# Kernel optimization log

Hardware: AMD Instinct MI355X
Metric: run time of the kernel (lower is better)

The kernel has to match this reference:

```python
import jax, jax.numpy as jnp
import numpy as np

P, N, M, B = 5, 30000, 50000, 256
T, C, L, ED, H, EMB, TD, NL = 13, 16, 3, 4, 128, 64, 5, 3
SRC = jnp.repeat(jnp.arange(P), P)  # edge type i = src*P + dst
DST = jnp.tile(jnp.arange(P), P)


def _affine(x, W, b):
    # x: [P, n, i], W: [P, i, o], b: [P, o]
    return jnp.einsum('pni,pio->pno', x, W) + b[:, None, :]


def _lrelu(x, s=0.01):
    return jnp.where(x >= 0, x, s * x)


def _gat(h, W, a_s, a_d, We, a_e, b, edge_index, edge_attr):
    # h: [P, N, H]; per-edge-type GATConv (heads=1, no self loops) then hetero 'max' aggregation
    hs, hd = h[SRC], h[DST]                       # [25, N, H]
    xl = jnp.einsum('enh,ehf->enf', hs, W)        # transformed source features
    xr = jnp.einsum('enh,ehf->enf', hd, W)
    als = jnp.einsum('enf,ef->en', xl, a_s)
    ald = jnp.einsum('enf,ef->en', xr, a_d)

    def per_type(xl_e, als_e, ald_e, ea, We_e, ae_e, ei):
        src, dst = ei[0], ei[1]
        alpha = als_e[src] + ald_e[dst] + (ea @ We_e) @ ae_e
        alpha = jnp.where(alpha >= 0, alpha, 0.2 * alpha)  # GAT negative_slope=0.2
        amax = jax.ops.segment_max(alpha, dst, num_segments=N)
        ex = jnp.exp(alpha - amax[dst])
        den = jax.ops.segment_sum(ex, dst, num_segments=N)
        w = ex / (den[dst] + 1e-16)
        return jax.ops.segment_sum(w[:, None] * xl_e[src], dst, num_segments=N)

    out = jax.vmap(per_type)(xl, als, ald, edge_attr, We, a_e, edge_index)
    out = out + b[:, None, :]
    return out.reshape(P, P, N, H).max(axis=0)  # HeteroConv aggr='max' over source types


def setup_inputs():
    key = jax.random.key(0)
    ks = iter(jax.random.split(key, 64))
    def nrm(shape, s=1.0):
        return jax.random.normal(next(ks), shape, dtype=jnp.float32) * s
    w = 0.05
    inp = {
        'x': nrm((P, N, T)),
        'cond_x': nrm((P, N, C + L)),
        'edge_attr': nrm((P * P, M, ED)),
        'timesteps': jax.random.uniform(next(ks), (B,), dtype=jnp.float32),
        'te1_W': nrm((1, TD), w), 'te1_b': nrm((TD,), w),
        'te2_W': nrm((TD, TD), w), 'te2_b': nrm((TD,), w),
        'emb_W': nrm((P, T + L, EMB), w), 'emb_b': nrm((P, EMB), w),
        'cemb_W': nrm((P, C, EMB), w), 'cemb_b': nrm((P, EMB), w),
        'pa_W': nrm((P, 2 * EMB, 2 * EMB), w), 'pa_b': nrm((P, 2 * EMB), w),
        'pc_W': nrm((P, 2 * EMB, EMB), w), 'pc_b': nrm((P, EMB), w),
        'sl0_W': nrm((P, EMB + TD, H), w), 'sl0_b': nrm((P, H), w),
        'sl12_W': nrm((2, P, H + TD, H), w), 'sl12_b': nrm((2, P, H), w),
        'slout_W': nrm((P, H + TD, T), w), 'slout_b': nrm((P, T), w),
        'gat_W': nrm((NL, P * P, H, H), w), 'gat_as': nrm((NL, P * P, H), w),
        'gat_ad': nrm((NL, P * P, H), w), 'gat_We': nrm((NL, P * P, ED, H), w),
        'gat_ae': nrm((NL, P * P, H), w), 'gat_b': nrm((NL, P * P, H), w),
        'xc_W': nrm((NL, P, H, H // 2), w), 'xc_b': nrm((NL, P, H // 2), w),
        'cc_W': nrm((NL, P, H, H // 2), w), 'cc_b': nrm((NL, P, H // 2), w),
        'ca_W': nrm((NL, P, H, H), w), 'ca_b': nrm((NL, P, H), w),
        'batch_idx': jax.random.randint(next(ks), (P, N), 0, B),
        'edge_index': jax.random.randint(next(ks), (P * P, 2, M), 0, N),
    }
    return inp


def reference(x, cond_x, edge_attr, timesteps, te1_W, te1_b, te2_W, te2_b,
              emb_W, emb_b, cemb_W, cemb_b, pa_W, pa_b, pc_W, pc_b,
              sl0_W, sl0_b, sl12_W, sl12_b, slout_W, slout_b,
              gat_W, gat_as, gat_ad, gat_We, gat_ae, gat_b,
              xc_W, xc_b, cc_W, cc_b, ca_W, ca_b, batch_idx, edge_index):
    # time embedding: Linear(1,TD) -> SiLU -> Linear(TD,TD)
    temb = jax.nn.silu(timesteps[:, None] @ te1_W + te1_b) @ te2_W + te2_b  # [B, TD]
    cond, latent = cond_x[..., :C], cond_x[..., C:]
    h = _affine(jnp.concatenate([x, latent], -1), emb_W, emb_b)            # [P,N,EMB]
    ce = _affine(cond, cemb_W, cemb_b)
    h = jnp.concatenate([h, ce], -1)                                       # [P,N,2EMB]
    h = jax.nn.sigmoid(_affine(h, pa_W, pa_b)) * h                         # attention pooling
    h = _affine(h, pc_W, pc_b)                                             # [P,N,EMB]
    nt = temb[batch_idx]                                                   # [P,N,TD]
    h = jnp.concatenate([h, nt], -1)
    for l in range(NL):
        if l > 0:
            h = jnp.concatenate([h, nt], -1)
        Wl, bl = (sl0_W, sl0_b) if l == 0 else (sl12_W[l - 1], sl12_b[l - 1])
        h = _lrelu(_affine(h, Wl, bl))                                     # [P,N,H]
        comm = _lrelu(_gat(h, gat_W[l], gat_as[l], gat_ad[l], gat_We[l], gat_ae[l], gat_b[l], edge_index, edge_attr))
        h = jnp.concatenate([_affine(h, xc_W[l], xc_b[l]), _affine(comm, cc_W[l], cc_b[l])], -1)
        h = h + jax.nn.sigmoid(_affine(h, ca_W[l], ca_b[l])) * h
    h = jnp.concatenate([h, nt], -1)
    return _affine(h, slout_W, slout_b)                                    # [P,N,T]
```

## Files before the change

kernel.cpp:

```cpp
#include <hip/hip_runtime.h>
#include <cstdio>

using bf8 = __attribute__((ext_vector_type(8))) short;
using f4v = __attribute__((ext_vector_type(4))) float;
typedef unsigned short u16;
typedef unsigned int u32;

#define DEV __device__ __forceinline__

DEV float bf2f(u16 u){ return __uint_as_float(((u32)u) << 16); }
DEV u16 f2bf(float f){ u32 u = __float_as_uint(f); return (u16)((u + 0x7fffu + ((u >> 16) & 1u)) >> 16); }
DEV float sigm(float v){ return 1.f / (1.f + __expf(-v)); }

constexpr int P5 = 5, NN = 30000, MM = 50000, NE = 25, BB = 256;
constexpr int KC = 96;
constexpr int RS = KC * 2 + 16;
constexpr int RSA = 272;

__global__ void temb_k(const float* ts, const float* w1, const float* b1,
                       const float* w2, const float* b2, float* temb){
  int i = blockIdx.x * blockDim.x + threadIdx.x;
  if (i >= BB) return;
  float t = ts[i]; float z[5];
#pragma unroll
  for (int j = 0; j < 5; ++j){ float u = t * w1[j] + b1[j]; z[j] = u * sigm(u); }
#pragma unroll
  for (int j2 = 0; j2 < 5; ++j2){
    float s = b2[j2];
#pragma unroll
    for (int j = 0; j < 5; ++j) s += z[j] * w2[j * 5 + j2];
    temb[i * 5 + j2] = s;
  }
}

__global__ void wtransE_k(const float* __restrict__ W, u16* __restrict__ Wt,
                          int Kreal, int Kpad, int Nreal, int Nalloc, int total){
  int idx = blockIdx.x * blockDim.x + threadIdx.x;
  if (idx >= total) return;
  int k = idx % Kpad;
  int t2 = idx / Kpad;
  int f = t2 % Nalloc;
  int b = t2 / Nalloc;
  float v = (k < Kreal && f < Nreal) ? W[((size_t)b * Kreal + k) * Nreal + f] : 0.f;
  Wt[idx] = f2bf(v);
}

__global__ void embw_k(const float* emb_W, const float* emb_b, const float* cemb_W, const float* cemb_b,
                       u16* Wc, float* bc){
  int b = blockIdx.x, f = threadIdx.x;
  for (int k = 0; k < 32; ++k){
    float v = 0.f;
    if (f < 64){ if (k < 16) v = emb_W[((size_t)b * 16 + k) * 64 + f]; }
    else       { if (k >= 16) v = cemb_W[((size_t)b * 16 + (k - 16)) * 64 + (f - 64)]; }
    Wc[((size_t)b * 128 + f) * 32 + k] = f2bf(v);
  }
  bc[b * 128 + f] = (f < 64) ? emb_b[b * 64 + f] : cemb_b[b * 64 + (f - 64)];
}

__global__ void gwtT_k(const float* __restrict__ gW, u16* __restrict__ gWt){
  int idx = blockIdx.x * blockDim.x + threadIdx.x;
  if (idx >= 75 * 128 * 128) return;
  int h = idx & 127, f = (idx >> 7) & 127, le = idx >> 14;
  gWt[idx] = f2bf(gW[(size_t)le * 16384 + h * 128 + f]);
}

__global__ void gatred_k(const float* gW, const float* gas, const float* gad,
                         const float* gWe, const float* gae,
                         float* wswd, float* eaw){
  int le = blockIdx.x; int h = threadIdx.x;
  const float* W = gW + (size_t)le * 16384;
  const float* as_ = gas + le * 128;
  const float* ad_ = gad + le * 128;
  float wsv = 0.f, wdv = 0.f;
  for (int f = 0; f < 128; ++f){
    float w = W[h * 128 + f];
    wsv += w * as_[f]; wdv += w * ad_[f];
  }
  wswd[le * 256 + h] = wsv;
  wswd[le * 256 + 128 + h] = wdv;
  if (h < 4){
    const float* We = gWe + (size_t)le * 512;
    const float* ae = gae + le * 128;
    float s = 0.f;
    for (int f = 0; f < 128; ++f) s += We[h * 128 + f] * ae[f];
    eaw[le * 4 + h] = s;
  }
}

__global__ void abuild_k(const float* x, const float* cx, u16* A0){
  int idx = blockIdx.x * blockDim.x + threadIdx.x;
  if (idx >= P5 * NN) return;
  const float* xr = x + (size_t)idx * 13;
  const float* cr = cx + (size_t)idx * 19;
  u16* a0 = A0 + (size_t)idx * 32;
#pragma unroll
  for (int i = 0; i < 13; ++i) a0[i] = f2bf(xr[i]);
#pragma unroll
  for (int i = 0; i < 3; ++i) a0[13 + i] = f2bf(cr[16 + i]);
#pragma unroll
  for (int i = 0; i < 16; ++i) a0[16 + i] = f2bf(cr[i]);
}

__global__ void ntfill_k(u16* buf, int pitch, int co, const int* bidx, const float* temb){
  int idx = blockIdx.x * blockDim.x + threadIdx.x;
  if (idx >= P5 * NN) return;
  int b = bidx[idx];
  u16* r = buf + (size_t)idx * pitch;
#pragma unroll
  for (int j = 0; j < 5; ++j) r[co + j] = f2bf(temb[b * 5 + j]);
  for (int j = co + 5; j < pitch; ++j) r[j] = 0;
}

__global__ __launch_bounds__(1024) void csr_build_k(const int* __restrict__ EI, int* __restrict__ off,
                                                    int* __restrict__ mpos, int* __restrict__ srcC){
  extern __shared__ int cntl[];
  __shared__ int wsum[16];
  int e = blockIdx.x, tid = threadIdx.x;
  int lane = tid & 63, wv = tid >> 6;
  for (int i = tid; i < NN; i += 1024) cntl[i] = 0;
  __syncthreads();
  const int* srcp = EI + (size_t)e * 2 * MM;
  const int* dstp = srcp + MM;
  for (int m = tid; m < MM; m += 1024) atomicAdd(&cntl[dstp[m]], 1);
  __syncthreads();
  int running = 0;
  for (int c = 0; c < 30; ++c){
    int idx = c * 1024 + tid;
    int v = (idx < NN) ? cntl[idx] : 0;
    int s = v;
#pragma unroll
    for (int o = 1; o < 64; o <<= 1){ int t = __shfl_up(s, o, 64); if (lane >= o) s += t; }
    if (lane == 63) wsum[wv] = s;
    __syncthreads();
    if (wv == 0 && lane < 16){
      int t = wsum[lane];
#pragma unroll
      for (int o = 1; o < 16; o <<= 1){ int u = __shfl_up(t, o, 64); if (lane >= o) t += u; }
      wsum[lane] = t;
    }
    __syncthreads();
    int base = running + ((wv > 0) ? wsum[wv - 1] : 0);
    int ex = base + s - v;
    if (idx < NN){ off[(size_t)e * (NN + 1) + idx] = ex; cntl[idx] = ex; }
    running += wsum[15];
    __syncthreads();
  }
  if (tid == 0) off[(size_t)e * (NN + 1) + NN] = running;
  __syncthreads();
  for (int m = tid; m < MM; m += 1024){
    int d = dstp[m];
    int pos = atomicAdd(&cntl[d], 1);
    mpos[(size_t)e * MM + m] = pos;
    srcC[(size_t)e * MM + pos] = srcp[m];
  }
}

__global__ void eadot_k(const float* __restrict__ ea, const float* __restrict__ eaw,
                        const int* __restrict__ mpos, float* __restrict__ eadot){
  int idx = blockIdx.x * blockDim.x + threadIdx.x;
  if (idx >= 3 * NE * MM) return;
  int l = idx / (NE * MM);
  int rem = idx - l * NE * MM;
  int e = rem / MM, m = rem - e * MM;
  const float* a4 = ea + ((size_t)e * MM + m) * 4;
  const float* ew = eaw + (size_t)(l * NE + e) * 4;
  float d = a4[0] * ew[0] + a4[1] * ew[1] + a4[2] * ew[2] + a4[3] * ew[3];
  eadot[(size_t)l * NE * MM + (size_t)e * MM + mpos[rem]] = d;
}

__global__ __launch_bounds__(256) void dots2_k(const u16* __restrict__ hS, const float* __restrict__ wswd_l,
                                               float* __restrict__ als, float* __restrict__ ald){
  __shared__ u32 hl[64][65];
  __shared__ float wsl[10][129];
  int p = blockIdx.y;
  int n0 = blockIdx.x * 64;
  int tid = threadIdx.x;
  for (int i = tid; i < 10 * 128; i += 256){
    int col = i >> 7, k = i & 127;
    int e = (col < 5) ? (p * 5 + col) : ((col - 5) * 5 + p);
    wsl[col][k] = wswd_l[e * 256 + ((col < 5) ? 0 : 128) + k];
  }
  for (int i = tid; i < 64 * 64; i += 256){
    int r = i >> 6, kp = i & 63;
    int n = n0 + r;
    hl[r][kp] = (n < NN) ? ((const u32*)hS)[((size_t)p * NN + n) * 64 + kp] : 0u;
  }
  __syncthreads();
  int col = tid & 15, rbase = tid >> 4;
  if (col < 10){
#pragma unroll
    for (int pass = 0; pass < 4; ++pass){
      int r = rbase + pass * 16;
      int n = n0 + r;
      if (n >= NN) continue;
      float s = 0.f;
#pragma unroll
      for (int kp = 0; kp < 64; ++kp){
        u32 pr = hl[r][kp];
        s += bf2f((u16)(pr & 0xffffu)) * wsl[col][2 * kp]
           + bf2f((u16)(pr >> 16)) * wsl[col][2 * kp + 1];
      }
      if (col < 5) als[(size_t)(p * 5 + col) * NN + n] = s;
      else         ald[(size_t)((col - 5) * 5 + p) * NN + n] = s;
    }
  }
}

__global__ __launch_bounds__(256) void aexp_k(const float* __restrict__ als, const float* __restrict__ ald,
                                              const float* __restrict__ eadot_l, const int* __restrict__ srcC,
                                              const int* __restrict__ off, uint2* __restrict__ prec){
  int idx = blockIdx.x * blockDim.x + threadIdx.x;
  if (idx >= NE * NN) return;
  int e = idx / NN;
  int ro = off[(size_t)e + idx], re = off[(size_t)e + idx + 1];
  if (ro >= re) return;
  float av = ald[idx];
  const int* sc = srcC + (size_t)e * MM;
  const float* ed = eadot_l + (size_t)e * MM;
  const float* ale = als + (size_t)e * NN;
  float mx = -3.0e38f;
  for (int j = ro; j < re; ++j){
    float a = ale[sc[j]] + av + ed[j];
    a = (a >= 0.f) ? a : 0.2f * a;
    mx = fmaxf(mx, a);
  }
  for (int j = ro; j < re; ++j){
    int src = sc[j];
    float a = ale[src] + av + ed[j];
    a = (a >= 0.f) ? a : 0.2f * a;
    uint2 pr; pr.x = (u32)src; pr.y = __float_as_uint(__expf(a - mx));
    prec[(size_t)e * MM + j] = pr;
  }
}

__global__ __launch_bounds__(256) void agg3_k(const u16* __restrict__ hS, const uint2* __restrict__ prec,
                                              const int* __restrict__ off, u16* __restrict__ agghB,
                                              int pd0, int npd){
  int l = threadIdx.x & 63, w = threadIdx.x >> 6;
  int n0 = blockIdx.x * 8 + w;
  int n1 = n0 + 4;
  int y = blockIdx.y;
  int ps = y / npd, e = ps * 5 + pd0 + (y - ps * npd);
  const uint2* pe = prec + (size_t)e * MM;
  const int* offe = off + (size_t)e * (NN + 1);
  const u32* hb = (const u32*)hS + (size_t)ps * NN * 64 + l;
  int ro0 = 0, ln0 = 0, ro1 = 0, ln1 = 0;
  if (n0 < NN){ ro0 = offe[n0]; ln0 = offe[n0 + 1] - ro0; }
  if (n1 < NN){ ro1 = offe[n1]; ln1 = offe[n1 + 1] - ro1; }
  float den0 = 0.f, a00 = 0.f, a01 = 0.f;
  float den1 = 0.f, a10 = 0.f, a11 = 0.f;
  int mx = (ln0 > ln1) ? ln0 : ln1;
  for (int t = 0; t < mx; ++t){
    if (t < ln0){
      uint2 pr = pe[ro0 + t];
      float ex = __uint_as_float(pr.y);
      u32 hv = hb[(size_t)pr.x * 64];
      den0 += ex; a00 += ex * bf2f((u16)(hv & 0xffffu)); a01 += ex * bf2f((u16)(hv >> 16));
    }
    if (t < ln1){
      uint2 pr = pe[ro1 + t];
      float ex = __uint_as_float(pr.y);
      u32 hv = hb[(size_t)pr.x * 64];
      den1 += ex; a10 += ex * bf2f((u16)(hv & 0xffffu)); a11 += ex * bf2f((u16)(hv >> 16));
    }
  }
  if (n0 < NN){
    float inv = 1.f / (den0 + 1e-16f);
    ((u32*)agghB)[((size_t)y * NN + n0) * 64 + l] = (u32)f2bf(a00 * inv) | ((u32)f2bf(a01 * inv) << 16);
  }
  if (n1 < NN){
    float inv = 1.f / (den1 + 1e-16f);
    ((u32*)agghB)[((size_t)y * NN + n1) * 64 + l] = (u32)f2bf(a10 * inv) | ((u32)f2bf(a11 * inv) << 16);
  }
}

template<int NF, int MI, int NJ, int EPI, bool ALRELU>
__global__ __launch_bounds__(256) void tgemm_k(const u16* __restrict__ A, const u16* __restrict__ Wt,
                                               const float* __restrict__ bias, void* __restrict__ out,
                                               const u16* __restrict__ X,
                                               int Kpad, int opitch, int ocol, int xpitch){
  constexpr int Nalloc = NF * 16;
  constexpr int WR = 128 / (MI * 16);
  constexpr int WC = 4 / WR;
  static_assert(WR * WC == 4 && NJ * WC * 16 == Nalloc, "wave tiling");
  extern __shared__ __align__(16) char smem[];
  float* Cs = (float*)smem;
  const int tid = threadIdx.x;
  const int l = tid & 63, w = tid >> 6;
  const int bz = blockIdx.z;
  const int r0 = blockIdx.x * 128;
  const int wr = w / WC, wc = w % WC;
  const size_t Ab = (size_t)bz * NN;

  f4v acc[MI][NJ];
#pragma unroll
  for (int i = 0; i < MI; ++i)
#pragma unroll
    for (int j = 0; j < NJ; ++j) acc[i][j] = f4v{0.f, 0.f, 0.f, 0.f};

  for (int kb = 0; kb < Kpad; kb += KC){
    int kc = Kpad - kb; if (kc > KC) kc = KC;
    int nseg = kc >> 3;
    for (int s = tid; s < 128 * nseg; s += 256){
      int r = s / nseg, c = s - r * nseg;
      int grow = r0 + r; if (grow > NN - 1) grow = NN - 1;
      uint4 v = *(const uint4*)(A + (Ab + grow) * Kpad + kb + c * 8);
      if (ALRELU){
        u32 pr[4] = {v.x, v.y, v.z, v.w};
#pragma unroll
        for (int q = 0; q < 4; ++q){
          float lo = bf2f((u16)(pr[q] & 0xffffu)), hi = bf2f((u16)(pr[q] >> 16));
          lo = lo >= 0.f ? lo : 0.01f * lo; hi = hi >= 0.f ? hi : 0.01f * hi;
          pr[q] = (u32)f2bf(lo) | ((u32)f2bf(hi) << 16);
        }
        v.x = pr[0]; v.y = pr[1]; v.z = pr[2]; v.w = pr[3];
      }
      *(uint4*)(smem + r * RS + c * 16) = v;
    }
    for (int s = tid; s < Nalloc * nseg; s += 256){
      int r = s / nseg, c = s - r * nseg;
      uint4 v = *(const uint4*)(Wt + ((size_t)bz * Nalloc + r) * Kpad + kb + c * 8);
      *(uint4*)(smem + 128 * RS + r * RS + c * 16) = v;
    }
    __syncthreads();
    int KI = kc >> 5;
    for (int k0 = 0; k0 < KI; ++k0){
      bf8 af[MI], bfr[NJ];
#pragma unroll
      for (int i = 0; i < MI; ++i){
        int row = wr * (MI * 16) + i * 16 + (l & 15);
        af[i] = *(const bf8*)(smem + row * RS + k0 * 64 + (l >> 4) * 16);
      }
#pragma unroll
      for (int j = 0; j < NJ; ++j){
        int col = wc * (NJ * 16) + j * 16 + (l & 15);
        bfr[j] = *(const bf8*)(smem + 128 * RS + col * RS + k0 * 64 + (l >> 4) * 16);
      }
#pragma unroll
      for (int i = 0; i < MI; ++i)
#pragma unroll
        for (int j = 0; j < NJ; ++j)
          acc[i][j] = __builtin_amdgcn_mfma_f32_16x16x32_bf16(af[i], bfr[j], acc[i][j], 0, 0, 0);
    }
    __syncthreads();
  }

  if (EPI == 4){
    int col = l & 15;
    if (col < 13){
#pragma unroll
      for (int i = 0; i < MI; ++i){
        float bv = bias[bz * 13 + col];
#pragma unroll
        for (int r = 0; r < 4; ++r){
          int grow = r0 + wr * (MI * 16) + i * 16 + (l >> 4) * 4 + r;
          if (grow < NN)
            ((float*)out)[((size_t)bz * NN + grow) * 13 + col] = acc[i][0][r] + bv;
        }
      }
    }
    return;
  }

#pragma unroll
  for (int i = 0; i < MI; ++i)
#pragma unroll
    for (int j = 0; j < NJ; ++j){
      int tcol = wc * (NJ * 16) + j * 16 + (l & 15);
      float bv = bias[bz * Nalloc + tcol];
#pragma unroll
      for (int r = 0; r < 4; ++r){
        int trow = wr * (MI * 16) + i * 16 + (l >> 4) * 4 + r;
        float v = acc[i][j][r] + bv;
        if (EPI == 2) v = v >= 0.f ? v : 0.01f * v;
        Cs[trow * Nalloc + tcol] = v;
      }
    }
  __syncthreads();
  constexpr int nsc = Nalloc / 4;
  u16* o16 = (u16*)out;
  for (int s = tid; s < 128 * nsc; s += 256){
    int r = s / nsc, c = s - r * nsc;
    int grow = r0 + r; if (grow >= NN) continue;
    float4 cv = *(const float4*)(Cs + r * Nalloc + c * 4);
    float v0 = cv.x, v1 = cv.y, v2 = cv.z, v3 = cv.w;
    if (EPI == 1){
      uint2 xv = *(const uint2*)(X + ((size_t)bz * NN + grow) * xpitch + c * 4);
      float x0 = bf2f((u16)(xv.x & 0xffffu)), x1 = bf2f((u16)(xv.x >> 16));
      float x2 = bf2f((u16)(xv.y & 0xffffu)), x3 = bf2f((u16)(xv.y >> 16));
      v0 = x0 * sigm(v0); v1 = x1 * sigm(v1); v2 = x2 * sigm(v2); v3 = x3 * sigm(v3);
    }
    uint2 ov;
    ov.x = (u32)f2bf(v0) | ((u32)f2bf(v1) << 16);
    ov.y = (u32)f2bf(v2) | ((u32)f2bf(v3) << 16);
    *(uint2*)(o16 + ((size_t)bz * NN + grow) * opitch + ocol + c * 4) = ov;
  }
}

__global__ __launch_bounds__(256) void tgatmm_k(const u16* __restrict__ agghB, const u16* __restrict__ gWt_l,
                                                const float* __restrict__ gb_l, u16* __restrict__ comm,
                                                int pd){
  extern __shared__ __align__(16) char smem[];
  char* As = smem;
  char* Bs = smem + 128 * RSA;
  float* Cs = (float*)smem;
  const int tid = threadIdx.x, l = tid & 63, w = tid >> 6;
  const int r0 = blockIdx.x * 128;
  const int wr = w >> 1, wc = w & 1;
  f4v vmax[4][4];
#pragma unroll 1
  for (int ps = 0; ps < 5; ++ps){
    int e = ps * 5 + pd;
    const u16* aggs = agghB + (size_t)ps * NN * 128;
    const u16* wb = gWt_l + (size_t)e * 16384;
    for (int s = tid; s < 128 * 16; s += 256){
      int r = s >> 4, c = s & 15;
      int grow = r0 + r; if (grow > NN - 1) grow = NN - 1;
      *(uint4*)(As + r * RSA + c * 16) = *(const uint4*)(aggs + (size_t)grow * 128 + c * 8);
      *(uint4*)(Bs + r * RSA + c * 16) = *(const uint4*)(wb + r * 128 + c * 8);
    }
    __syncthreads();
    f4v acc[4][4];
#pragma unroll
    for (int i = 0; i < 4; ++i)
#pragma unroll
      for (int j = 0; j < 4; ++j) acc[i][j] = f4v{0.f, 0.f, 0.f, 0.f};
#pragma unroll
    for (int k0 = 0; k0 < 4; ++k0){
      bf8 af[4], bfr[4];
#pragma unroll
      for (int i = 0; i < 4; ++i)
        af[i] = *(const bf8*)(As + (wr * 64 + i * 16 + (l & 15)) * RSA + k0 * 64 + (l >> 4) * 16);
#pragma unroll
      for (int j = 0; j < 4; ++j)
        bfr[j] = *(const bf8*)(Bs + (wc * 64 + j * 16 + (l & 15)) * RSA + k0 * 64 + (l >> 4) * 16);
#pragma unroll
      for (int i = 0; i < 4; ++i)
#pragma unroll
        for (int j = 0; j < 4; ++j)
          acc[i][j] = __builtin_amdgcn_mfma_f32_16x16x32_bf16(af[i], bfr[j], acc[i][j], 0, 0, 0);
    }
    const float* be = gb_l + e * 128;
#pragma unroll
    for (int i = 0; i < 4; ++i)
#pragma unroll
      for (int j = 0; j < 4; ++j){
        int tcol = wc * 64 + j * 16 + (l & 15);
        float bv = be[tcol];
#pragma unroll
        for (int r = 0; r < 4; ++r){
          float cvv = acc[i][j][r] + bv;
          vmax[i][j][r] = (ps == 0) ? cvv : fmaxf(vmax[i][j][r], cvv);
        }
      }
    __syncthreads();
  }
#pragma unroll
  for (int i = 0; i < 4; ++i)
#pragma unroll
    for (int j = 0; j < 4; ++j){
      int tcol = wc * 64 + j * 16 + (l & 15);
#pragma unroll
      for (int r = 0; r < 4; ++r){
        int trow = wr * 64 + i * 16 + (l >> 4) * 4 + r;
        Cs[trow * 128 + tcol] = vmax[i][j][r];
      }
    }
  __syncthreads();
  for (int s = tid; s < 128 * 32; s += 256){
    int r = s >> 5, c = s & 31;
    int grow = r0 + r; if (grow >= NN) continue;
    float4 cv = *(const float4*)(Cs + r * 128 + c * 4);
    uint2 ov;
    ov.x = (u32)f2bf(cv.x) | ((u32)f2bf(cv.y) << 16);
    ov.y = (u32)f2bf(cv.z) | ((u32)f2bf(cv.w) << 16);
    *(uint2*)(comm + ((size_t)pd * NN + grow) * 128 + c * 4) = ov;
  }
}

__global__ __launch_bounds__(512) void fca_k(const u16* __restrict__ hS, const u16* __restrict__ comm,
                                             const u16* __restrict__ wxc_l, const float* __restrict__ bxc_l,
                                             const u16* __restrict__ wcc_l, const float* __restrict__ bcc_l,
                                             const u16* __restrict__ wca_l, const float* __restrict__ bca_l,
                                             u16* __restrict__ hL){
  extern __shared__ __align__(16) char smem[];
  char* As = smem;
  char* H2 = smem + 128 * RSA;
  const int tid = threadIdx.x, l = tid & 63, wv = tid >> 6;
  const int wr = wv >> 1, wc = wv & 1;
  const int bz = blockIdx.z;
  const int r0 = blockIdx.x * 128;
  const size_t pb = (size_t)bz * NN;

  f4v acc_a[2][2], acc_b[2][2];
  for (int s = tid; s < 128 * 16; s += 512){
    int r = s >> 4, c = s & 15;
    int grow = r0 + r; if (grow > NN - 1) grow = NN - 1;
    *(uint4*)(As + r * RSA + c * 16) = *(const uint4*)(hS + (pb + grow) * 128 + c * 8);
  }
  for (int s = tid; s < 64 * 16; s += 512){
    int r = s >> 4, c = s & 15;
    *(uint4*)(H2 + r * RSA + c * 16) = *(const uint4*)(wxc_l + (size_t)bz * 8192 + r * 128 + c * 8);
  }
  __syncthreads();
#pragma unroll
  for (int i = 0; i < 2; ++i)
#pragma unroll
    for (int j = 0; j < 2; ++j) acc_a[i][j] = f4v{0.f, 0.f, 0.f, 0.f};
#pragma unroll
  for (int k0 = 0; k0 < 4; ++k0){
    bf8 af[2], bfr[2];
#pragma unroll
    for (int i = 0; i < 2; ++i)
      af[i] = *(const bf8*)(As + (wr * 32 + i * 16 + (l & 15)) * RSA + k0 * 64 + (l >> 4) * 16);
#pragma unroll
    for (int j = 0; j < 2; ++j)
      bfr[j] = *(const bf8*)(H2 + (wc * 32 + j * 16 + (l & 15)) * RSA + k0 * 64 + (l >> 4) * 16);
#pragma unroll
    for (int i = 0; i < 2; ++i)
#pragma unroll
      for (int j = 0; j < 2; ++j)
        acc_a[i][j] = __builtin_amdgcn_mfma_f32_16x16x32_bf16(af[i], bfr[j], acc_a[i][j], 0, 0, 0);
  }
  __syncthreads();
  for (int s = tid; s < 128 * 16; s += 512){
    int r = s >> 4, c = s & 15;
    int grow = r0 + r; if (grow > NN - 1) grow = NN - 1;
    uint4 v = *(const uint4*)(comm + (pb + grow) * 128 + c * 8);
    u32 pr[4] = {v.x, v.y, v.z, v.w};
#pragma unroll
    for (int q = 0; q < 4; ++q){
      float lo = bf2f((u16)(pr[q] & 0xffffu)), hi = bf2f((u16)(pr[q] >> 16));
      lo = lo >= 0.f ? lo : 0.01f * lo; hi = hi >= 0.f ? hi : 0.01f * hi;
      pr[q] = (u32)f2bf(lo) | ((u32)f2bf(hi) << 16);
    }
    v.x = pr[0]; v.y = pr[1]; v.z = pr[2]; v.w = pr[3];
    *(uint4*)(As + r * RSA + c * 16) = v;
  }
  for (int s = tid; s < 64 * 16; s += 512){
    int r = s >> 4, c = s & 15;
    *(uint4*)(H2 + r * RSA + c * 16) = *(const uint4*)(wcc_l + (size_t)bz * 8192 + r * 128 + c * 8);
  }
  __syncthreads();
#pragma unroll
  for (int i = 0; i < 2; ++i)
#pragma unroll
    for (int j = 0; j < 2; ++j) acc_b[i][j] = f4v{0.f, 0.f, 0.f, 0.f};
#pragma unroll
  for (int k0 = 0; k0 < 4; ++k0){
    bf8 af[2], bfr[2];
#pragma unroll
    for (int i = 0; i < 2; ++i)
      af[i] = *(const bf8*)(As + (wr * 32 + i * 16 + (l & 15)) * RSA + k0 * 64 + (l >> 4) * 16);
#pragma unroll
    for (int j = 0; j < 2; ++j)
      bfr[j] = *(const bf8*)(H2 + (wc * 32 + j * 16 + (l & 15)) * RSA + k0 * 64 + (l >> 4) * 16);
#pragma unroll
    for (int i = 0; i < 2; ++i)
#pragma unroll
      for (int j = 0; j < 2; ++j)
        acc_b[i][j] = __builtin_amdgcn_mfma_f32_16x16x32_bf16(af[i], bfr[j], acc_b[i][j], 0, 0, 0);
  }
  __syncthreads();
#pragma unroll
  for (int i = 0; i < 2; ++i)
#pragma unroll
    for (int j = 0; j < 2; ++j){
      int colL = wc * 32 + j * 16 + (l & 15);
      float bL = bxc_l[bz * 64 + colL];
      float bR = bcc_l[bz * 64 + colL];
#pragma unroll
      for (int r = 0; r < 4; ++r){
        int row = wr * 32 + i * 16 + (l >> 4) * 4 + r;
        *(u16*)(H2 + row * RSA + colL * 2)       = f2bf(acc_a[i][j][r] + bL);
        *(u16*)(H2 + row * RSA + (colL + 64) * 2) = f2bf(acc_b[i][j][r] + bR);
      }
    }
  for (int s = tid; s < 128 * 16; s += 512){
    int r = s >> 4, c = s & 15;
    *(uint4*)(As + r * RSA + c * 16) = *(const uint4*)(wca_l + (size_t)bz * 16384 + r * 128 + c * 8);
  }
  __syncthreads();
  f4v acc_g[2][4];
#pragma unroll
  for (int i = 0; i < 2; ++i)
#pragma unroll
    for (int j = 0; j < 4; ++j) acc_g[i][j] = f4v{0.f, 0.f, 0.f, 0.f};
#pragma unroll
  for (int k0 = 0; k0 < 4; ++k0){
    bf8 af[2], bfr[4];
#pragma unroll
    for (int i = 0; i < 2; ++i)
      af[i] = *(const bf8*)(H2 + (wr * 32 + i * 16 + (l & 15)) * RSA + k0 * 64 + (l >> 4) * 16);
#pragma unroll
    for (int j = 0; j < 4; ++j)
      bfr[j] = *(const bf8*)(As + (wc * 64 + j * 16 + (l & 15)) * RSA + k0 * 64 + (l >> 4) * 16);
#pragma unroll
    for (int i = 0; i < 2; ++i)
#pragma unroll
      for (int j = 0; j < 4; ++j)
        acc_g[i][j] = __builtin_amdgcn_mfma_f32_16x16x32_bf16(af[i], bfr[j], acc_g[i][j], 0, 0, 0);
  }
  float vout[2][4][4];
#pragma unroll
  for (int i = 0; i < 2; ++i)
#pragma unroll
    for (int j = 0; j < 4; ++j){
      int col = wc * 64 + j * 16 + (l & 15);
      float bv = bca_l[bz * 128 + col];
#pragma unroll
      for (int r = 0; r < 4; ++r){
        int row = wr * 32 + i * 16 + (l >> 4) * 4 + r;
        float xg = bf2f(*(const u16*)(H2 + row * RSA + col * 2));
        vout[i][j][r] = xg * (1.f + sigm(acc_g[i][j][r] + bv));
      }
    }
  __syncthreads();
#pragma unroll
  for (int i = 0; i < 2; ++i)
#pragma unroll
    for (int j = 0; j < 4; ++j){
      int col = wc * 64 + j * 16 + (l & 15);
#pragma unroll
      for (int r = 0; r < 4; ++r){
        int row = wr * 32 + i * 16 + (l >> 4) * 4 + r;
        *(u16*)(H2 + row * RSA + col * 2) = f2bf(vout[i][j][r]);
      }
    }
  __syncthreads();
  for (int s = tid; s < 128 * 32; s += 512){
    int r = s >> 5, c = s & 31;
    int grow = r0 + r; if (grow >= NN) continue;
    uint2 v = *(const uint2*)(H2 + r * RSA + c * 8);
    *(uint2*)(hL + (pb + grow) * 160 + c * 4) = v;
  }
}

constexpr size_t ALN(size_t x){ return (x + 255) & ~(size_t)255; }
constexpr size_t SZ_A0   = ALN((size_t)P5 * NN * 32 * 2);
constexpr size_t SZ_H0   = ALN((size_t)P5 * NN * 96 * 2);
constexpr size_t SZ_H128 = ALN((size_t)P5 * NN * 128 * 2);
constexpr size_t SZ_HL   = ALN((size_t)P5 * NN * 160 * 2);
constexpr size_t O_A0 = 0;
constexpr size_t O_H0 = O_A0 + SZ_A0;
constexpr size_t O_AGG = 0;
constexpr size_t O_HCAT = O_H0 + SZ_H0;
constexpr size_t O_HG = O_HCAT + SZ_H128;
constexpr size_t O_HS = O_HG + SZ_H128;
constexpr size_t O_HL = O_HS + SZ_H128;
constexpr size_t O_TEMB = O_HL + SZ_HL;
constexpr size_t O_WSWD = O_TEMB + ALN(256 * 5 * 4);
constexpr size_t O_EAW  = O_WSWD + ALN(75 * 256 * 4);
constexpr size_t O_OFFS = O_EAW + ALN(75 * 4 * 4);
constexpr size_t O_MPOS = O_OFFS + ALN((size_t)NE * (NN + 1) * 4);
constexpr size_t O_ALS  = O_MPOS + ALN((size_t)NE * MM * 4);
constexpr size_t O_ALD  = O_ALS + ALN((size_t)NE * NN * 4);
constexpr size_t O_SRCC = O_ALD + ALN((size_t)NE * NN * 4);
constexpr size_t O_EADOT= O_SRCC + ALN((size_t)NE * MM * 4);
constexpr size_t O_GWT  = O_EADOT + ALN((size_t)3 * NE * MM * 4);
constexpr size_t O_WCMB = O_GWT + ALN((size_t)75 * 16384 * 2);
constexpr size_t O_BCMB = O_WCMB + ALN((size_t)5 * 128 * 32 * 2);
constexpr size_t O_WPA  = O_BCMB + ALN((size_t)5 * 128 * 4);
constexpr size_t O_WPC  = O_WPA + ALN((size_t)5 * 128 * 128 * 2);
constexpr size_t O_WSL0 = O_WPC + ALN((size_t)5 * 64 * 128 * 2);
constexpr size_t O_WSL12= O_WSL0 + ALN((size_t)5 * 128 * 96 * 2);
constexpr size_t O_WSLO = O_WSL12 + ALN((size_t)10 * 128 * 160 * 2);
constexpr size_t O_WXC  = O_WSLO + ALN((size_t)5 * 16 * 160 * 2);
constexpr size_t O_WCC  = O_WXC + ALN((size_t)15 * 64 * 128 * 2);
constexpr size_t O_WCA  = O_WCC + ALN((size_t)15 * 64 * 128 * 2);
constexpr size_t O_PREC = O_WCA + ALN((size_t)15 * 128 * 128 * 2);
constexpr size_t WS_NEED= O_PREC + ALN((size_t)NE * MM * 8);

extern "C" void kernel_launch(void* const* d_in, const int* in_sizes, int n_in,
                              void* d_out, int out_size, void* d_ws, size_t ws_size,
                              hipStream_t stream){
  if (ws_size < WS_NEED){
    fprintf(stderr, "kernel_launch: ws too small: need %zu have %zu\n", WS_NEED, ws_size);
    return;
  }
  const float* x        = (const float*)d_in[0];
  const float* cond_x   = (const float*)d_in[1];
  const float* edge_attr= (const float*)d_in[2];
  const float* timesteps= (const float*)d_in[3];
  const float* te1_W = (const float*)d_in[4];
  const float* te1_b = (const float*)d_in[5];
  const float* te2_W = (const float*)d_in[6];
  const float* te2_b = (const float*)d_in[7];
  const float* emb_W = (const float*)d_in[8];
  const float* emb_b = (const float*)d_in[9];
  const float* cemb_W= (const float*)d_in[10];
  const float* cemb_b= (const float*)d_in[11];
  const float* pa_W  = (const float*)d_in[12];
  const float* pa_b  = (const float*)d_in[13];
  const float* pc_W  = (const float*)d_in[14];
  const float* pc_b  = (const float*)d_in[15];
  const float* sl0_W = (const float*)d_in[16];
  const float* sl0_b = (const float*)d_in[17];
  const float* sl12_W= (const float*)d_in[18];
  const float* sl12_b= (const float*)d_in[19];
  const float* slout_W=(const float*)d_in[20];
  const float* slout_b=(const float*)d_in[21];
  const float* gat_W = (const float*)d_in[22];
  const float* gat_as= (const float*)d_in[23];
  const float* gat_ad= (const float*)d_in[24];
  const float* gat_We= (const float*)d_in[25];
  const float* gat_ae= (const float*)d_in[26];
  const float* gat_b = (const float*)d_in[27];
  const float* xc_W  = (const float*)d_in[28];
  const float* xc_b  = (const float*)d_in[29];
  const float* cc_W  = (const float*)d_in[30];
  const float* cc_b  = (const float*)d_in[31];
  const float* ca_W  = (const float*)d_in[32];
  const float* ca_b  = (const float*)d_in[33];
  const int* batch_idx = (const int*)d_in[34];
  const int* edge_index= (const int*)d_in[35];

  char* ws = (char*)d_ws;
  u16* A0    = (u16*)(ws + O_A0);
  u16* h0buf = (u16*)(ws + O_H0);
  u16* agghB = (u16*)(ws + O_AGG);
  u16* hcat  = (u16*)(ws + O_HCAT);
  u16* hg    = (u16*)(ws + O_HG);
  u16* comm  = (u16*)(ws + O_HG);
  u16* hS    = (u16*)(ws + O_HS);
  u16* hL    = (u16*)(ws + O_HL);
  float* tembp = (float*)(ws + O_TEMB);
  float* wswdp = (float*)(ws + O_WSWD);
  float* eawp  = (float*)(ws + O_EAW);
  int* offs = (int*)(ws + O_OFFS);
  int* mposp= (int*)(ws + O_MPOS);
  float* alsp = (float*)(ws + O_ALS);
  float* aldp = (float*)(ws + O_ALD);
  int* srcCp = (int*)(ws + O_SRCC);
  float* eadotp = (float*)(ws + O_EADOT);
  u16* gwt   = (u16*)(ws + O_GWT);
  u16* wcmb  = (u16*)(ws + O_WCMB);
  float* bcmb= (float*)(ws + O_BCMB);
  u16* wpa   = (u16*)(ws + O_WPA);
  u16* wpc   = (u16*)(ws + O_WPC);
  u16* wsl0  = (u16*)(ws + O_WSL0);
  u16* wsl12 = (u16*)(ws + O_WSL12);
  u16* wslo  = (u16*)(ws + O_WSLO);
  u16* wxc   = (u16*)(ws + O_WXC);
  u16* wcc   = (u16*)(ws + O_WCC);
  u16* wca   = (u16*)(ws + O_WCA);
  uint2* precp = (uint2*)(ws + O_PREC);

  const dim3 B256(256);
  const dim3 TG(235, 1, 5);
  const int GPN = (P5 * NN + 255) / 256;
  const int GEN = (NE * NN + 255) / 256;
  constexpr int LDS_N128 = 65536;
  constexpr int LDS_N64  = 39936;
  constexpr int LDS_SLO  = 29952;
  constexpr int LDS_TGAT = 128 * RSA * 2;
  constexpr int LDS_FCA  = 128 * RSA * 2;
  constexpr int LDS_CSR  = NN * 4;

  temb_k<<<1, B256, 0, stream>>>(timesteps, te1_W, te1_b, te2_W, te2_b, tembp);
  embw_k<<<5, 128, 0, stream>>>(emb_W, emb_b, cemb_W, cemb_b, wcmb, bcmb);
  {
    auto WT = [&](const float* W, u16* Wt, int Kr, int Kp, int Nr, int Na, int B){
      int total = B * Na * Kp;
      wtransE_k<<<(total + 255) / 256, B256, 0, stream>>>(W, Wt, Kr, Kp, Nr, Na, total);
    };
    WT(pa_W, wpa, 128, 128, 128, 128, 5);
    WT(pc_W, wpc, 128, 128, 64, 64, 5);
    WT(sl0_W, wsl0, 69, 96, 128, 128, 5);
    WT(sl12_W, wsl12, 133, 160, 128, 128, 10);
    WT(slout_W, wslo, 133, 160, 13, 16, 5);
    WT(xc_W, wxc, 128, 128, 64, 64, 15);
    WT(cc_W, wcc, 128, 128, 64, 64, 15);
    WT(ca_W, wca, 128, 128, 128, 128, 15);
  }
  gwtT_k<<<(75 * 128 * 128 + 255) / 256, B256, 0, stream>>>(gat_W, gwt);
  gatred_k<<<75, 128, 0, stream>>>(gat_W, gat_as, gat_ad, gat_We, gat_ae, wswdp, eawp);

  csr_build_k<<<25, 1024, LDS_CSR, stream>>>(edge_index, offs, mposp, srcCp);
  eadot_k<<<(3 * NE * MM + 255) / 256, B256, 0, stream>>>(edge_attr, eawp, mposp, eadotp);

  abuild_k<<<GPN, B256, 0, stream>>>(x, cond_x, A0);
  tgemm_k<8, 4, 4, 0, false><<<TG, B256, LDS_N128, stream>>>(A0, wcmb, bcmb, hcat, nullptr, 32, 128, 0, 0);
  tgemm_k<8, 4, 4, 1, false><<<TG, B256, LDS_N128, stream>>>(hcat, wpa, pa_b, hg, hcat, 128, 128, 0, 128);
  tgemm_k<4, 2, 4, 0, false><<<TG, B256, LDS_N64, stream>>>(hg, wpc, pc_b, h0buf, nullptr, 128, 96, 0, 0);
  ntfill_k<<<GPN, B256, 0, stream>>>(h0buf, 96, 64, batch_idx, tembp);

  for (int l = 0; l < 3; ++l){
    if (l == 0)
      tgemm_k<8, 4, 4, 2, false><<<TG, B256, LDS_N128, stream>>>(h0buf, wsl0, sl0_b, hS, nullptr, 96, 128, 0, 0);
    else
      tgemm_k<8, 4, 4, 2, false><<<TG, B256, LDS_N128, stream>>>(hL, wsl12 + (size_t)(l - 1) * 5 * 128 * 160,
                                                                 sl12_b + (size_t)(l - 1) * 5 * 128, hS, nullptr,
                                                                 160, 128, 0, 0);
    const float* wswd_l = wswdp + (size_t)l * 25 * 256;
    const u16* gwt_l = gwt + (size_t)l * 25 * 16384;
    const float* gb_l = gat_b + (size_t)l * 25 * 128;
    dots2_k<<<dim3(469, 5), B256, 0, stream>>>(hS, wswd_l, alsp, aldp);
    aexp_k<<<GEN, B256, 0, stream>>>(alsp, aldp, eadotp + (size_t)l * NE * MM, srcCp, offs, precp);
    for (int pd = 0; pd < 5; ++pd){
      agg3_k<<<dim3(3750, 5), B256, 0, stream>>>(hS, precp, offs, agghB, pd, 1);
      tgatmm_k<<<dim3(235), B256, LDS_TGAT, stream>>>(agghB, gwt_l, gb_l, comm, pd);
    }
    fca_k<<<dim3(235, 1, 5), 512, LDS_FCA, stream>>>(hS, comm,
        wxc + (size_t)l * 5 * 64 * 128, xc_b + (size_t)l * 5 * 64,
        wcc + (size_t)l * 5 * 64 * 128, cc_b + (size_t)l * 5 * 64,
        wca + (size_t)l * 5 * 128 * 128, ca_b + (size_t)l * 5 * 128, hL);
    ntfill_k<<<GPN, B256, 0, stream>>>(hL, 160, 128, batch_idx, tembp);
  }

  tgemm_k<1, 2, 1, 4, false><<<TG, B256, LDS_SLO, stream>>>(hL, wslo, slout_b, d_out, nullptr, 160, 13, 0, 0);
}
```

Before: 1.821 ms.

## Fuse edge-attr dot into CSR build, halve tgatmm tiles, fuse ntfill into fca

The edge-attribute dot products are now computed inside csr_build_k at the scatter position, which removes the mpos buffer and the separate eadot kernel. The CSR prefix scan becomes a single-pass per-thread serial scan over 30 counts each. tgatmm_k now uses 64-row tiles with twice as many blocks, for better occupancy on 256 CUs. The time-embedding fill of hL is folded into the fca epilogue, dropping three ntfill launches. The serial per-thread scan gives strided LDS access, and the smaller GEMM tiles reload the weight tile more often.

```diff
diff --git a/kernel.cpp b/kernel.cpp
--- a/kernel.cpp
+++ b/kernel.cpp
@@ -111,8 +111,10 @@
   for (int j = co + 5; j < pitch; ++j) r[j] = 0;
 }
 
-__global__ __launch_bounds__(1024) void csr_build_k(const int* __restrict__ EI, int* __restrict__ off,
-                                                    int* __restrict__ mpos, int* __restrict__ srcC){
+__global__ __launch_bounds__(1024) void csr_build_k(const int* __restrict__ EI, const float* __restrict__ ea,
+                                                    const float* __restrict__ eaw,
+                                                    int* __restrict__ off, int* __restrict__ srcC,
+                                                    float* __restrict__ eadot){
   extern __shared__ int cntl[];
   __shared__ int wsum[16];
   int e = blockIdx.x, tid = threadIdx.x;
@@ -123,49 +125,44 @@
   const int* dstp = srcp + MM;
   for (int m = tid; m < MM; m += 1024) atomicAdd(&cntl[dstp[m]], 1);
   __syncthreads();
-  int running = 0;
-  for (int c = 0; c < 30; ++c){
-    int idx = c * 1024 + tid;
-    int v = (idx < NN) ? cntl[idx] : 0;
-    int s = v;
-#pragma unroll
-    for (int o = 1; o < 64; o <<= 1){ int t = __shfl_up(s, o, 64); if (lane >= o) s += t; }
-    if (lane == 63) wsum[wv] = s;
-    __syncthreads();
-    if (wv == 0 && lane < 16){
-      int t = wsum[lane];
-#pragma unroll
-      for (int o = 1; o < 16; o <<= 1){ int u = __shfl_up(t, o, 64); if (lane >= o) t += u; }
-      wsum[lane] = t;
-    }
-    __syncthreads();
-    int base = running + ((wv > 0) ? wsum[wv - 1] : 0);
-    int ex = base + s - v;
-    if (idx < NN){ off[(size_t)e * (NN + 1) + idx] = ex; cntl[idx] = ex; }
-    running += wsum[15];
-    __syncthreads();
-  }
-  if (tid == 0) off[(size_t)e * (NN + 1) + NN] = running;
-  __syncthreads();
+  int t0 = tid * 30, t1 = t0 + 30;
+  if (t0 > NN) t0 = NN;
+  if (t1 > NN) t1 = NN;
+  int tsum = 0;
+  for (int i = t0; i < t1; ++i) tsum += cntl[i];
+  int s = tsum;
+#pragma unroll
+  for (int o = 1; o < 64; o <<= 1){ int t = __shfl_up(s, o, 64); if (lane >= o) s += t; }
+  if (lane == 63) wsum[wv] = s;
+  __syncthreads();
+  if (wv == 0 && lane < 16){
+    int t = wsum[lane];
+#pragma unroll
+    for (int o = 1; o < 16; o <<= 1){ int u = __shfl_up(t, o, 64); if (lane >= o) t += u; }
+    wsum[lane] = t;
+  }
+  __syncthreads();
+  int run = ((wv > 0) ? wsum[wv - 1] : 0) + (s - tsum);
+  for (int i = t0; i < t1; ++i){
+    int v = cntl[i];
+    off[(size_t)e * (NN + 1) + i] = run;
+    cntl[i] = run;
+    run += v;
+  }
+  if (tid == 0) off[(size_t)e * (NN + 1) + NN] = wsum[15];
+  __syncthreads();
+  float4 ew0 = *(const float4*)(eaw + (size_t)(0 * NE + e) * 4);
+  float4 ew1 = *(const float4*)(eaw + (size_t)(1 * NE + e) * 4);
+  float4 ew2 = *(const float4*)(eaw + (size_t)(2 * NE + e) * 4);
   for (int m = tid; m < MM; m += 1024){
     int d = dstp[m];
     int pos = atomicAdd(&cntl[d], 1);
-    mpos[(size_t)e * MM + m] = pos;
     srcC[(size_t)e * MM + pos] = srcp[m];
-  }
-}
-
-__global__ void eadot_k(const float* __restrict__ ea, const float* __restrict__ eaw,
-                        const int* __restrict__ mpos, float* __restrict__ eadot){
-  int idx = blockIdx.x * blockDim.x + threadIdx.x;
-  if (idx >= 3 * NE * MM) return;
-  int l = idx / (NE * MM);
-  int rem = idx - l * NE * MM;
-  int e = rem / MM, m = rem - e * MM;
-  const float* a4 = ea + ((size_t)e * MM + m) * 4;
-  const float* ew = eaw + (size_t)(l * NE + e) * 4;
-  float d = a4[0] * ew[0] + a4[1] * ew[1] + a4[2] * ew[2] + a4[3] * ew[3];
-  eadot[(size_t)l * NE * MM + (size_t)e * MM + mpos[rem]] = d;
+    float4 a4 = *(const float4*)(ea + ((size_t)e * MM + m) * 4);
+    eadot[(size_t)e * MM + pos]                          = a4.x * ew0.x + a4.y * ew0.y + a4.z * ew0.z + a4.w * ew0.w;
+    eadot[(size_t)NE * MM + (size_t)e * MM + pos]        = a4.x * ew1.x + a4.y * ew1.y + a4.z * ew1.z + a4.w * ew1.w;
+    eadot[(size_t)2 * NE * MM + (size_t)e * MM + pos]    = a4.x * ew2.x + a4.y * ew2.y + a4.z * ew2.z + a4.w * ew2.w;
+  }
 }
 
 __global__ __launch_bounds__(256) void dots2_k(const u16* __restrict__ hS, const float* __restrict__ wswd_l,
@@ -402,47 +399,50 @@
                                                 int pd){
   extern __shared__ __align__(16) char smem[];
   char* As = smem;
-  char* Bs = smem + 128 * RSA;
+  char* Bs = smem + 64 * RSA;
   float* Cs = (float*)smem;
   const int tid = threadIdx.x, l = tid & 63, w = tid >> 6;
-  const int r0 = blockIdx.x * 128;
+  const int r0 = blockIdx.x * 64;
   const int wr = w >> 1, wc = w & 1;
-  f4v vmax[4][4];
+  f4v vmax[2][4];
 #pragma unroll 1
   for (int ps = 0; ps < 5; ++ps){
     int e = ps * 5 + pd;
     const u16* aggs = agghB + (size_t)ps * NN * 128;
     const u16* wb = gWt_l + (size_t)e * 16384;
-    for (int s = tid; s < 128 * 16; s += 256){
+    for (int s = tid; s < 64 * 16; s += 256){
       int r = s >> 4, c = s & 15;
       int grow = r0 + r; if (grow > NN - 1) grow = NN - 1;
       *(uint4*)(As + r * RSA + c * 16) = *(const uint4*)(aggs + (size_t)grow * 128 + c * 8);
+    }
+    for (int s = tid; s < 128 * 16; s += 256){
+      int r = s >> 4, c = s & 15;
       *(uint4*)(Bs + r * RSA + c * 16) = *(const uint4*)(wb + r * 128 + c * 8);
     }
     __syncthreads();
-    f4v acc[4][4];
-#pragma unroll
-    for (int i = 0; i < 4; ++i)
+    f4v acc[2][4];
+#pragma unroll
+    for (int i = 0; i < 2; ++i)
 #pragma unroll
       for (int j = 0; j < 4; ++j) acc[i][j] = f4v{0.f, 0.f, 0.f, 0.f};
 #pragma unroll
     for (int k0 = 0; k0 < 4; ++k0){
-      bf8 af[4], bfr[4];
-#pragma unroll
-      for (int i = 0; i < 4; ++i)
-        af[i] = *(const bf8*)(As + (wr * 64 + i * 16 + (l & 15)) * RSA + k0 * 64 + (l >> 4) * 16);
+      bf8 af[2], bfr[4];
+#pragma unroll
+      for (int i = 0; i < 2; ++i)
+        af[i] = *(const bf8*)(As + (wr * 32 + i * 16 + (l & 15)) * RSA + k0 * 64 + (l >> 4) * 16);
 #pragma unroll
       for (int j = 0; j < 4; ++j)
         bfr[j] = *(const bf8*)(Bs + (wc * 64 + j * 16 + (l & 15)) * RSA + k0 * 64 + (l >> 4) * 16);
 #pragma unroll
-      for (int i = 0; i < 4; ++i)
+      for (int i = 0; i < 2; ++i)
 #pragma unroll
         for (int j = 0; j < 4; ++j)
           acc[i][j] = __builtin_amdgcn_mfma_f32_16x16x32_bf16(af[i], bfr[j], acc[i][j], 0, 0, 0);
     }
     const float* be = gb_l + e * 128;
 #pragma unroll
-    for (int i = 0; i < 4; ++i)
+    for (int i = 0; i < 2; ++i)
 #pragma unroll
       for (int j = 0; j < 4; ++j){
         int tcol = wc * 64 + j * 16 + (l & 15);
@@ -456,18 +456,18 @@
     __syncthreads();
   }
 #pragma unroll
-  for (int i = 0; i < 4; ++i)
+  for (int i = 0; i < 2; ++i)
 #pragma unroll
     for (int j = 0; j < 4; ++j){
       int tcol = wc * 64 + j * 16 + (l & 15);
 #pragma unroll
       for (int r = 0; r < 4; ++r){
-        int trow = wr * 64 + i * 16 + (l >> 4) * 4 + r;
+        int trow = wr * 32 + i * 16 + (l >> 4) * 4 + r;
         Cs[trow * 128 + tcol] = vmax[i][j][r];
       }
     }
   __syncthreads();
-  for (int s = tid; s < 128 * 32; s += 256){
+  for (int s = tid; s < 64 * 32; s += 256){
     int r = s >> 5, c = s & 31;
     int grow = r0 + r; if (grow >= NN) continue;
     float4 cv = *(const float4*)(Cs + r * 128 + c * 4);
@@ -482,6 +482,7 @@
                                              const u16* __restrict__ wxc_l, const float* __restrict__ bxc_l,
                                              const u16* __restrict__ wcc_l, const float* __restrict__ bcc_l,
                                              const u16* __restrict__ wca_l, const float* __restrict__ bca_l,
+                                             const int* __restrict__ bidx, const float* __restrict__ temb,
                                              u16* __restrict__ hL){
   extern __shared__ __align__(16) char smem[];
   char* As = smem;
@@ -572,7 +573,7 @@
 #pragma unroll
       for (int r = 0; r < 4; ++r){
         int row = wr * 32 + i * 16 + (l >> 4) * 4 + r;
-        *(u16*)(H2 + row * RSA + colL * 2)       = f2bf(acc_a[i][j][r] + bL);
+        *(u16*)(H2 + row * RSA + colL * 2)        = f2bf(acc_a[i][j][r] + bL);
         *(u16*)(H2 + row * RSA + (colL + 64) * 2) = f2bf(acc_b[i][j][r] + bR);
       }
     }
@@ -628,11 +629,26 @@
       }
     }
   __syncthreads();
-  for (int s = tid; s < 128 * 32; s += 512){
-    int r = s >> 5, c = s & 31;
+  for (int s = tid; s < 128 * 40; s += 512){
+    int r = s / 40, c = s - r * 40;
     int grow = r0 + r; if (grow >= NN) continue;
-    uint2 v = *(const uint2*)(H2 + r * RSA + c * 8);
-    *(uint2*)(hL + (pb + grow) * 160 + c * 4) = v;
+    if (c < 32){
+      uint2 v = *(const uint2*)(H2 + r * RSA + c * 8);
+      *(uint2*)(hL + (pb + grow) * 160 + c * 4) = v;
+    } else {
+      int b = bidx[pb + grow];
+      int col0 = c * 4;
+      u16 t[4];
+#pragma unroll
+      for (int q = 0; q < 4; ++q){
+        int j = col0 + q - 128;
+        t[q] = (j < 5) ? f2bf(temb[b * 5 + j]) : (u16)0;
+      }
+      uint2 ov;
+      ov.x = (u32)t[0] | ((u32)t[1] << 16);
+      ov.y = (u32)t[2] | ((u32)t[3] << 16);
+      *(uint2*)(hL + (pb + grow) * 160 + col0) = ov;
+    }
   }
 }
 
@@ -652,8 +668,7 @@
 constexpr size_t O_WSWD = O_TEMB + ALN(256 * 5 * 4);
 constexpr size_t O_EAW  = O_WSWD + ALN(75 * 256 * 4);
 constexpr size_t O_OFFS = O_EAW + ALN(75 * 4 * 4);
-constexpr size_t O_MPOS = O_OFFS + ALN((size_t)NE * (NN + 1) * 4);
-constexpr size_t O_ALS  = O_MPOS + ALN((size_t)NE * MM * 4);
+constexpr size_t O_ALS  = O_OFFS + ALN((size_t)NE * (NN + 1) * 4);
 constexpr size_t O_ALD  = O_ALS + ALN((size_t)NE * NN * 4);
 constexpr size_t O_SRCC = O_ALD + ALN((size_t)NE * NN * 4);
 constexpr size_t O_EADOT= O_SRCC + ALN((size_t)NE * MM * 4);
@@ -728,7 +743,6 @@
   float* wswdp = (float*)(ws + O_WSWD);
   float* eawp  = (float*)(ws + O_EAW);
   int* offs = (int*)(ws + O_OFFS);
-  int* mposp= (int*)(ws + O_MPOS);
   float* alsp = (float*)(ws + O_ALS);
   float* aldp = (float*)(ws + O_ALD);
   int* srcCp = (int*)(ws + O_SRCC);
@@ -753,7 +767,7 @@
   constexpr int LDS_N128 = 65536;
   constexpr int LDS_N64  = 39936;
   constexpr int LDS_SLO  = 29952;
-  constexpr int LDS_TGAT = 128 * RSA * 2;
+  constexpr int LDS_TGAT = 64 * RSA + 128 * RSA;
   constexpr int LDS_FCA  = 128 * RSA * 2;
   constexpr int LDS_CSR  = NN * 4;
 
@@ -776,8 +790,7 @@
   gwtT_k<<<(75 * 128 * 128 + 255) / 256, B256, 0, stream>>>(gat_W, gwt);
   gatred_k<<<75, 128, 0, stream>>>(gat_W, gat_as, gat_ad, gat_We, gat_ae, wswdp, eawp);
 
-  csr_build_k<<<25, 1024, LDS_CSR, stream>>>(edge_index, offs, mposp, srcCp);
-  eadot_k<<<(3 * NE * MM + 255) / 256, B256, 0, stream>>>(edge_attr, eawp, mposp, eadotp);
+  csr_build_k<<<25, 1024, LDS_CSR, stream>>>(edge_index, edge_attr, eawp, offs, srcCp, eadotp);
 
   abuild_k<<<GPN, B256, 0, stream>>>(x, cond_x, A0);
   tgemm_k<8, 4, 4, 0, false><<<TG, B256, LDS_N128, stream>>>(A0, wcmb, bcmb, hcat, nullptr, 32, 128, 0, 0);
@@ -799,13 +812,13 @@
     aexp_k<<<GEN, B256, 0, stream>>>(alsp, aldp, eadotp + (size_t)l * NE * MM, srcCp, offs, precp);
     for (int pd = 0; pd < 5; ++pd){
       agg3_k<<<dim3(3750, 5), B256, 0, stream>>>(hS, precp, offs, agghB, pd, 1);
-      tgatmm_k<<<dim3(235), B256, LDS_TGAT, stream>>>(agghB, gwt_l, gb_l, comm, pd);
+      tgatmm_k<<<dim3(469), B256, LDS_TGAT, stream>>>(agghB, gwt_l, gb_l, comm, pd);
     }
     fca_k<<<dim3(235, 1, 5), 512, LDS_FCA, stream>>>(hS, comm,
         wxc + (size_t)l * 5 * 64 * 128, xc_b + (size_t)l * 5 * 64,
         wcc + (size_t)l * 5 * 64 * 128, cc_b + (size_t)l * 5 * 64,
-        wca + (size_t)l * 5 * 128 * 128, ca_b + (size_t)l * 5 * 128, hL);
-    ntfill_k<<<GPN, B256, 0, stream>>>(hL, 160, 128, batch_idx, tembp);
+        wca + (size_t)l * 5 * 128 * 128, ca_b + (size_t)l * 5 * 128,
+        batch_idx, tembp, hL);
   }
 
   tgemm_k<1, 2, 1, 4, false><<<TG, B256, LDS_SLO, stream>>>(hL, wslo, slout_b, d_out, nullptr, 160, 13, 0, 0);
```

New measurement: 1.962 ms. 7.8% more time.
